# Kernel tuning notes

Hardware: AMD Instinct MI355X
Metric: run time of the kernel (lower is better)

## Reference

```python
import jax, jax.numpy as jnp
import numpy as np

Q, N, D = 4096, 100000, 128


def setup_inputs() -> dict:
    key = jax.random.key(0)
    k1, k2, k3 = jax.random.split(key, 3)
    inputs = jax.random.normal(k1, (Q, D), dtype=jnp.float32)
    X_train = jax.random.normal(k2, (N, D), dtype=jnp.float32)
    y_train = jax.random.normal(k3, (N,), dtype=jnp.float32)
    return {"inputs": inputs, "X_train": X_train, "y_train": y_train, "k": 32}


def reference(inputs, X_train, y_train, k):
    # Squared Euclidean distances [Q, N] via the expanded identity
    # |a-b|^2 = |a|^2 + |b|^2 - 2 a.b  (avoids materializing [Q, N, D]).
    q_sq = jnp.sum(inputs * inputs, axis=-1, keepdims=True)        # [Q, 1]
    t_sq = jnp.sum(X_train * X_train, axis=-1)                     # [N]
    cross = jnp.einsum('qd,nd->qn', inputs, X_train)               # [Q, N]
    distances = q_sq + t_sq[None, :] - 2.0 * cross                 # [Q, N]
    # top_k of -distances == k nearest neighbors
    _, indices = jax.lax.top_k(-distances, k)                      # [Q, k]
    nearest = y_train[indices]                                     # [Q, k]
    return jnp.mean(nearest, axis=1)                               # [Q]
```

## Files before the change

### kernel.cpp

```cpp
#include <hip/hip_runtime.h>
#include <hip/hip_fp16.h>
#include <cstdint>
#include <cstddef>


constexpr int Q_  = 4096;
constexpr int N_  = 100000;
constexpr int D_  = 128;
constexpr int K_  = 32;

constexpr int QT    = 32;
constexpr int BN    = 256;
constexpr int NCH   = 8;
constexpr int CHUNK = 12544;
constexpr int ITERS = CHUNK / BN;
constexpr int NPAD  = NCH * CHUNK;
constexpr int CW    = 128;
constexpr int QTS   = 16;
constexpr int SAMP_M      = 8192;
constexpr int SAMP_STRIDE = 12;
constexpr int SAMP_OFF    = 5;
constexpr int SAMP_ITERS  = SAMP_M / BN;

constexpr int XS_B  = NPAD / 64;
constexpr int SAM_B = SAMP_M / 64;
constexpr int PQ_B  = Q_ / 4;
constexpr int MXN   = XS_B * 4;

typedef __attribute__((ext_vector_type(8))) _Float16 half8;
typedef __attribute__((ext_vector_type(4))) float    floatx4;
typedef unsigned long long ull;

#define DEV __device__ __forceinline__
constexpr ull DEADC = ~0ull;

DEV ull pack_cand(float score, unsigned int n) {
    unsigned int s = __float_as_uint(score);
    s = (s & 0x80000000u) ? ~s : (s | 0x80000000u);
    return ((ull)s << 32) | (ull)n;
}
DEV float unpack_score(ull k) {
    unsigned int s = (unsigned int)(k >> 32);
    s = (s & 0x80000000u) ? (s ^ 0x80000000u) : ~s;
    return __uint_as_float(s);
}
DEV ull u64min(ull a, ull b) { return a < b ? a : b; }
DEV float inf_f() { return __int_as_float(0x7f800000); }

DEV ull bitonic64(ull v, int L) {
    #pragma unroll
    for (int k2 = 2; k2 <= 64; k2 <<= 1)
        #pragma unroll
        for (int j2 = k2 >> 1; j2 >= 1; j2 >>= 1) {
            ull o = __shfl_xor(v, j2);
            bool up = ((L & k2) == 0);
            bool lo = ((L & j2) == 0);
            ull mn = u64min(v, o), mx = v ^ o ^ mn;
            v = (lo == up) ? mn : mx;
        }
    return v;
}
DEV ull bimerge64(ull v, int L) {
    #pragma unroll
    for (int j2 = 32; j2 >= 1; j2 >>= 1) {
        ull o = __shfl_xor(v, j2);
        ull mn = u64min(v, o), mx = v ^ o ^ mn;
        v = ((L & j2) == 0) ? mn : mx;
    }
    return v;
}

__global__ void prep_all(const float* __restrict__ X, const float* __restrict__ Qm,
                         __half* __restrict__ Xs, float* __restrict__ tsq,
                         float* __restrict__ mxArr, float* __restrict__ mxArrH,
                         __half* __restrict__ Xsam, float* __restrict__ tsqS,
                         __half* __restrict__ Qh,
                         float* __restrict__ qsq, float* __restrict__ qrs,
                         int* __restrict__ flagF)
{
    const int tid = threadIdx.x, L = tid & 63, wv = tid >> 6;
    const int bx = blockIdx.x;
    const int am = L & 15, aq = L >> 4;

    if (bx < XS_B) {
        int t16 = bx * 4 + wv;
        int r = t16 * 16 + am;
        float ssq = 0.f, xr2 = 0.f, xh2 = 0.f;
        #pragma unroll
        for (int ks = 0; ks < 4; ++ks) {
            int c = ks * 32 + aq * 8;
            float v0=0,v1=0,v2=0,v3=0,v4=0,v5=0,v6=0,v7=0;
            if (r < N_) {
                float4 a = *(const float4*)(X + (size_t)r * D_ + c);
                float4 b = *(const float4*)(X + (size_t)r * D_ + c + 4);
                v0=a.x; v1=a.y; v2=a.z; v3=a.w; v4=b.x; v5=b.y; v6=b.z; v7=b.w;
            }
            half8 h;
            h[0]=(_Float16)v0; h[1]=(_Float16)v1; h[2]=(_Float16)v2; h[3]=(_Float16)v3;
            h[4]=(_Float16)v4; h[5]=(_Float16)v5; h[6]=(_Float16)v6; h[7]=(_Float16)v7;
            float c0=(float)h[0], c1=(float)h[1], c2=(float)h[2], c3=(float)h[3];
            float c4=(float)h[4], c5=(float)h[5], c6=(float)h[6], c7=(float)h[7];
            float r0=v0-c0, r1=v1-c1, r2=v2-c2, r3=v3-c3;
            float r4=v4-c4, r5=v5-c5, r6=v6-c6, r7=v7-c7;
            ssq += v0*v0+v1*v1+v2*v2+v3*v3+v4*v4+v5*v5+v6*v6+v7*v7;
            xr2 += r0*r0+r1*r1+r2*r2+r3*r3+r4*r4+r5*r5+r6*r6+r7*r7;
            xh2 += c0*c0+c1*c1+c2*c2+c3*c3+c4*c4+c5*c5+c6*c6+c7*c7;
            *(half8*)(Xs + ((size_t)(t16 * 4 + ks)) * 512 + L * 8) = h;
        }
        ssq += __shfl_xor(ssq, 16); ssq += __shfl_xor(ssq, 32);
        xr2 += __shfl_xor(xr2, 16); xr2 += __shfl_xor(xr2, 32);
        xh2 += __shfl_xor(xh2, 16); xh2 += __shfl_xor(xh2, 32);
        if (aq == 0) tsq[r] = (r < N_) ? ssq : inf_f();
        float m = xr2;
        m = fmaxf(m, __shfl_xor(m, 1)); m = fmaxf(m, __shfl_xor(m, 2));
        m = fmaxf(m, __shfl_xor(m, 4)); m = fmaxf(m, __shfl_xor(m, 8));
        float mh = xh2;
        mh = fmaxf(mh, __shfl_xor(mh, 1)); mh = fmaxf(mh, __shfl_xor(mh, 2));
        mh = fmaxf(mh, __shfl_xor(mh, 4)); mh = fmaxf(mh, __shfl_xor(mh, 8));
        if (L == 0) { mxArr[t16] = m; mxArrH[t16] = mh; }
    } else if (bx < XS_B + SAM_B) {
        int t16 = (bx - XS_B) * 4 + wv;
        int j = t16 * 16 + am;
        int n = j * SAMP_STRIDE + SAMP_OFF;
        float ssq = 0.f;
        #pragma unroll
        for (int ks = 0; ks < 4; ++ks) {
            int c = ks * 32 + aq * 8;
            float4 a = *(const float4*)(X + (size_t)n * D_ + c);
            float4 b = *(const float4*)(X + (size_t)n * D_ + c + 4);
            half8 h;
            h[0]=(_Float16)a.x; h[1]=(_Float16)a.y; h[2]=(_Float16)a.z; h[3]=(_Float16)a.w;
            h[4]=(_Float16)b.x; h[5]=(_Float16)b.y; h[6]=(_Float16)b.z; h[7]=(_Float16)b.w;
            ssq += a.x*a.x + a.y*a.y + a.z*a.z + a.w*a.w
                 + b.x*b.x + b.y*b.y + b.z*b.z + b.w*b.w;
            *(half8*)(Xsam + ((size_t)(t16 * 4 + ks)) * 512 + L * 8) = h;
        }
        ssq += __shfl_xor(ssq, 16); ssq += __shfl_xor(ssq, 32);
        if (aq == 0) tsqS[j] = ssq;
    } else {
        int r = (bx - XS_B - SAM_B) * 4 + wv;
        float2 x = *(const float2*)(Qm + (size_t)r * D_ + 2 * L);
        __half h0 = __float2half(x.x), h1 = __float2half(x.y);
        size_t o = (size_t)r * D_ + 2 * L;
        Qh[o] = h0; Qh[o + 1] = h1;
        float r0 = x.x - __half2float(h0), r1 = x.y - __half2float(h1);
        float s  = x.x * x.x + x.y * x.y;
        float sr = r0 * r0 + r1 * r1;
        s  += __shfl_xor(s, 32);  s += __shfl_xor(s, 16);  s += __shfl_xor(s, 8);
        s  += __shfl_xor(s, 4);   s += __shfl_xor(s, 2);   s += __shfl_xor(s, 1);
        sr += __shfl_xor(sr, 32); sr += __shfl_xor(sr, 16); sr += __shfl_xor(sr, 8);
        sr += __shfl_xor(sr, 4);  sr += __shfl_xor(sr, 2);  sr += __shfl_xor(sr, 1);
        if (L == 0) { qsq[r] = s; qrs[r] = sr; flagF[r] = 0; }
    }
}

__global__ void reduce_mx(const float* __restrict__ mxArr,
                          const float* __restrict__ mxArrH,
                          float* __restrict__ mxOut)
{
    __shared__ float sR[4], sH[4];
    const int tid = threadIdx.x, L = tid & 63, wv = tid >> 6;
    float a = 0.f, b = 0.f;
    #pragma unroll 1
    for (int i = tid; i < MXN; i += 256) {
        a = fmaxf(a, mxArr[i]);
        b = fmaxf(b, mxArrH[i]);
    }
    #pragma unroll
    for (int s = 32; s; s >>= 1) {
        a = fmaxf(a, __shfl_xor(a, s));
        b = fmaxf(b, __shfl_xor(b, s));
    }
    if (L == 0) { sR[wv] = a; sH[wv] = b; }
    __syncthreads();
    if (tid == 0) {
        mxOut[0] = fmaxf(fmaxf(sR[0], sR[1]), fmaxf(sR[2], sR[3]));
        mxOut[1] = fmaxf(fmaxf(sH[0], sH[1]), fmaxf(sH[2], sH[3]));
    }
}

__global__ __launch_bounds__(256, 2) void sample_T(
    const __half* __restrict__ Qh, const __half* __restrict__ Xsam,
    const float* __restrict__ tsqS, const float* __restrict__ qsq,
    const float* __restrict__ qrs, const float* __restrict__ mxOut,
    float* __restrict__ Teff, float* __restrict__ rawT, float* __restrict__ EwA)
{
    __shared__ float sT[QTS][130];
    const int tid = threadIdx.x, L = tid & 63, wv = tid >> 6;
    const int qbase = blockIdx.x * QTS;
    const int nwv = wv * 64;
    const int am = L & 15, aq = L >> 4;

    half8 afh[4];
    #pragma unroll
    for (int ks = 0; ks < 4; ++ks) {
        size_t o = (size_t)(qbase + am) * D_ + ks * 32 + aq * 8;
        afh[ks] = *(const half8*)(Qh + o);
    }

    float t2a[4], t2b[4];
    #pragma unroll
    for (int rg = 0; rg < 4; ++rg) { t2a[rg] = inf_f(); t2b[rg] = inf_f(); }

    const __half* bp = Xsam + (size_t)nwv * 128 + (size_t)L * 8;
    const float*  tp = tsqS + nwv + am;

    half8 bc[4], bn[4];
    #pragma unroll
    for (int nt = 0; nt < 4; ++nt)
        bc[nt] = *(const half8*)(bp + nt * 2048);

    #pragma unroll 1
    for (int it = 0; it < SAMP_ITERS; ++it) {
        float ts[4];
        #pragma unroll
        for (int nt = 0; nt < 4; ++nt) ts[nt] = tp[nt * 16];

        floatx4 acc[4] = {};
        #pragma unroll
        for (int ks = 0; ks < 4; ++ks) {
            const __half* pp = (ks < 3) ? (bp + (ks + 1) * 512) : (bp + 32768);
            #pragma unroll
            for (int nt = 0; nt < 4; ++nt)
                bn[nt] = *(const half8*)(pp + nt * 2048);
            #pragma unroll
            for (int nt = 0; nt < 4; ++nt)
                acc[nt] = __builtin_amdgcn_mfma_f32_16x16x32_f16(
                    afh[ks], bc[nt], acc[nt], 0, 0, 0);
            #pragma unroll
            for (int nt = 0; nt < 4; ++nt) bc[nt] = bn[nt];
        }
        #pragma unroll
        for (int rg = 0; rg < 4; ++rg) {
            float m1 = t2a[rg], m2 = t2b[rg];
            #pragma unroll
            for (int nt = 0; nt < 4; ++nt) {
                float v = ts[nt] - 2.f * acc[nt][rg];
                if (v < m2) { if (v < m1) { m2 = m1; m1 = v; } else m2 = v; }
            }
            t2a[rg] = m1; t2b[rg] = m2;
        }
        bp += 32768; tp += BN;
    }
    #pragma unroll
    for (int rg = 0; rg < 4; ++rg) {
        int q = aq * 4 + rg;
        sT[q][wv * 32 + am * 2 + 0] = t2a[rg];
        sT[q][wv * 32 + am * 2 + 1] = t2b[rg];
    }
    __syncthreads();

    const float mxr = mxOut[0], mxh = mxOut[1];

    #pragma unroll 1
    for (int j = 0; j < 4; ++j) {
        int q = wv * 4 + j;
        float a = sT[q][2 * L], b = sT[q][2 * L + 1];
        float g = 0.f;
        #pragma unroll 1
        for (int r = 0; r < 16; ++r) {
            float mn = fminf(a, b);
            mn = fminf(mn, __shfl_xor(mn, 32)); mn = fminf(mn, __shfl_xor(mn, 16));
            mn = fminf(mn, __shfl_xor(mn, 8));  mn = fminf(mn, __shfl_xor(mn, 4));
            mn = fminf(mn, __shfl_xor(mn, 2));  mn = fminf(mn, __shfl_xor(mn, 1));
            g = mn;
            ull ba = __ballot(a == g);
            if (ba) { if (L == __ffsll(ba) - 1) a = inf_f(); }
            else    { ull bb = __ballot(b == g); if (L == __ffsll(bb) - 1) b = inf_f(); }
        }
        if (L == 0) {
            int gq = qbase + q;
            float e = 2.f * (sqrtf(qsq[gq]) * sqrtf(mxr)
                           + sqrtf(qrs[gq]) * sqrtf(mxh)) + 0.02f;
            rawT[gq] = g; EwA[gq] = e; Teff[gq] = g + e;
        }
    }
}

__global__ __launch_bounds__(256, 4) void knn_main(
    const __half* __restrict__ Qh, const __half* __restrict__ Xs,
    const float* __restrict__ tsq, const float* __restrict__ Teff,
    ull* __restrict__ candG, int* __restrict__ cntC, int* __restrict__ flagF)
{
    __shared__ ull candL[QT][CW];
    __shared__ int cntL[QT];

    const int tid = threadIdx.x, L = tid & 63, wv = tid >> 6;
    const int lb = blockIdx.x, ch = lb & 7;
    const int qbase = (lb >> 3) * QT, chBase = ch * CHUNK, nwv = wv * 64;
    const int am = L & 15, aq = L >> 4;

    if (tid < QT) cntL[tid] = 0;
    __syncthreads();

    float th[2][4];
    float nH[2];
    #pragma unroll
    for (int qt = 0; qt < 2; ++qt) {
        #pragma unroll
        for (int rg = 0; rg < 4; ++rg)
            th[qt][rg] = Teff[qbase + qt * 16 + aq * 4 + rg];
        float m = fmaxf(fmaxf(th[qt][0], th[qt][1]), fmaxf(th[qt][2], th[qt][3]));
        nH[qt] = -0.5f * m - 1e-3f;
    }

    half8 afh[2][4];
    #pragma unroll
    for (int qt = 0; qt < 2; ++qt)
        #pragma unroll
        for (int ks = 0; ks < 4; ++ks) {
            size_t o = (size_t)(qbase + qt * 16 + am) * D_ + ks * 32 + aq * 8;
            afh[qt][ks] = *(const half8*)(Qh + o);
        }

    const __half* bp = Xs + (size_t)(chBase + nwv) * 128 + (size_t)L * 8;
    const float*  tp = tsq + chBase + nwv + am;
    int n0 = chBase + nwv + am;

    half8 bc[4], bn[4];
    #pragma unroll
    for (int nt = 0; nt < 4; ++nt)
        bc[nt] = *(const half8*)(bp + nt * 2048);

    #pragma unroll 1
    for (int it = 0; it < ITERS; ++it) {
        float ts[4];
        #pragma unroll
        for (int nt = 0; nt < 4; ++nt) ts[nt] = tp[nt * 16];

        floatx4 acc[2][4] = {};
        #pragma unroll
        for (int ks = 0; ks < 4; ++ks) {
            const __half* pp = (ks < 3) ? (bp + (ks + 1) * 512) : (bp + 32768);
            #pragma unroll
            for (int nt = 0; nt < 4; ++nt)
                bn[nt] = *(const half8*)(pp + nt * 2048);
            #pragma unroll
            for (int nt = 0; nt < 4; ++nt) {
                acc[0][nt] = __builtin_amdgcn_mfma_f32_16x16x32_f16(
                    afh[0][ks], bc[nt], acc[0][nt], 0, 0, 0);
                acc[1][nt] = __builtin_amdgcn_mfma_f32_16x16x32_f16(
                    afh[1][ks], bc[nt], acc[1][nt], 0, 0, 0);
            }
            #pragma unroll
            for (int nt = 0; nt < 4; ++nt) bc[nt] = bn[nt];
        }

        unsigned hit = 0;
        #pragma unroll
        for (int nt = 0; nt < 4; ++nt) {
            #pragma unroll
            for (int qt = 0; qt < 2; ++qt) {
                float mx = fmaxf(fmaxf(acc[qt][nt][0], acc[qt][nt][1]),
                                 fmaxf(acc[qt][nt][2], acc[qt][nt][3]));
                float Gm = fmaf(0.5f, ts[nt], nH[qt]);
                if (mx > Gm) hit |= 1u << (nt * 2 + qt);
            }
        }
        if (__any(hit != 0)) {
            #pragma unroll
            for (int nt = 0; nt < 4; ++nt) {
                #pragma unroll
                for (int qt = 0; qt < 2; ++qt) {
                    if (!__any(hit & (1u << (nt * 2 + qt)))) continue;
                    unsigned n = (unsigned)(n0 + nt * 16);
                    #pragma unroll
                    for (int rg = 0; rg < 4; ++rg) {
                        float s = fmaf(-2.f, acc[qt][nt][rg], ts[nt]);
                        if (s < th[qt][rg]) {
                            int q = qt * 16 + aq * 4 + rg;
                            int pos = atomicAdd(&cntL[q], 1);
                            if (pos < CW)
                                candL[q][pos] = pack_cand(s, n);
                            else
                                flagF[qbase + q] = 1;
                        }
                    }
                }
            }
        }
        bp += 32768; tp += BN; n0 += BN;
    }

    __syncthreads();

    #pragma unroll 1
    for (int j = 0; j < 8; ++j) {
        int q = wv * 8 + j;
        int gq = qbase + q;
        int c = cntL[q];
        int cc = c < CW ? c : CW;
        ull* dst = candG + ((size_t)gq * NCH + ch) * CW;
        #pragma unroll
        for (int off = 0; off < CW; off += 64)
            if (off + L < cc) dst[off + L] = candL[q][off + L];
        if (L == 0) cntC[gq * NCH + ch] = cc;
    }
}

__global__ void finalize(const ull* __restrict__ candG, const int* __restrict__ cntC,
                         const int* __restrict__ flagF, const float* __restrict__ Qm,
                         const float* __restrict__ X, const float* __restrict__ tsq,
                         const float* __restrict__ rawT, const float* __restrict__ EwA,
                         const float* __restrict__ Ytr, float* __restrict__ out)
{
    __shared__ ull fb[4][256];
    int L = threadIdx.x & 63;
    int wv = threadIdx.x >> 6;
    int q = blockIdx.x * 4 + wv;
    bool bad = (flagF[q] != 0);
    float result = 0.f;

    if (!bad) {
        int cg = (L < NCH) ? cntC[q * NCH + L] : 0;
        int ctot = cg;
        ctot += __shfl_xor(ctot, 32); ctot += __shfl_xor(ctot, 16);
        ctot += __shfl_xor(ctot, 8);  ctot += __shfl_xor(ctot, 4);
        ctot += __shfl_xor(ctot, 2);  ctot += __shfl_xor(ctot, 1);
        if (ctot < K_) bad = true;
        else {
            ull s = DEADC;
            #pragma unroll 1
            for (int g = 0; g < NCH; ++g) {
                int c_g = __shfl(cg, g);
                const ull* cb = candG + ((size_t)q * NCH + g) * CW;
                #pragma unroll 1
                for (int off = 0; off < c_g; off += 64) {
                    ull v = (off + L < c_g) ? cb[off + L] : DEADC;
                    v = bitonic64(v, L);
                    ull w = __shfl(v, 63 - L);
                    s = bimerge64(u64min(s, w), L);
                }
            }
            int cr = ctot < 64 ? ctot : 64;
            unsigned n = (unsigned)(s & 0xffffffffu);
            ull pe = DEADC;
            if (L < cr) {
                const float4* xp = (const float4*)(X + (size_t)n * D_);
                const float4* qp = (const float4*)(Qm + (size_t)q * D_);
                float d = 0.f;
                #pragma unroll 8
                for (int i = 0; i < 32; ++i) {
                    float4 xv = xp[i], qv = qp[i];
                    d += qv.x * xv.x + qv.y * xv.y + qv.z * xv.z + qv.w * xv.w;
                }
                pe = pack_cand(tsq[n] - 2.f * d, n);
            }
            ull pe2 = bitonic64(pe, L);
            float exact31 = unpack_score(__shfl(pe2, K_ - 1));
            bool ok = exact31 < rawT[q];
            if (ctot > 64) {
                float A63 = unpack_score(__shfl(s, 63));
                ok = ok && (A63 - EwA[q] > exact31);
            }
            if (!ok) bad = true;
            else {
                float ys = 0.f;
                if (L < K_) ys = Ytr[(unsigned)(pe2 & 0xffffffffu)];
                ys += __shfl_xor(ys, 32); ys += __shfl_xor(ys, 16);
                ys += __shfl_xor(ys, 8);  ys += __shfl_xor(ys, 4);
                ys += __shfl_xor(ys, 2);  ys += __shfl_xor(ys, 1);
                result = ys * (1.f / K_);
            }
        }
    }

    if (bad) {
        const float4* qp = (const float4*)(Qm + (size_t)q * D_);
        float T = rawT[q] + EwA[q];
        float lo = 0.f, hi = 0.f;
        bool haveLo = false, haveHi = false;
        int cnt = 0;
        #pragma unroll 1
        for (int att = 0; att < 40; ++att) {
            cnt = 0;
            #pragma unroll 1
            for (int j = 0; j < NPAD / 64; ++j) {
                int n = j * 64 + L;
                float s = inf_f();
                if (n < N_) {
                    const float4* xp = (const float4*)(X + (size_t)n * D_);
                    float d = 0.f;
                    #pragma unroll 4
                    for (int i = 0; i < 32; ++i) {
                        float4 xv = xp[i], qv = qp[i];
                        d += qv.x * xv.x + qv.y * xv.y + qv.z * xv.z + qv.w * xv.w;
                    }
                    s = tsq[n] - 2.f * d;
                }
                bool want = s < T;
                ull m = __ballot(want);
                if (m) {
                    int pos = cnt + (int)__popcll(m & ((1ull << L) - 1ull));
                    if (want && pos < 256) fb[wv][pos] = pack_cand(s, (unsigned)n);
                    cnt += (int)__popcll(m);
                }
            }
            if (cnt >= K_ && cnt <= 256) break;
            if (cnt < K_) { lo = T; haveLo = true;
                T = haveHi ? 0.5f * (T + hi) : T + exp2f((float)att) * 0.5f; }
            else { hi = T; haveHi = true;
                T = haveLo ? 0.5f * (lo + T) : T - exp2f((float)att) * 0.5f; }
        }
        if (cnt >= K_ && cnt <= 256) {
            ull s64 = DEADC;
            #pragma unroll 1
            for (int off = 0; off < 256; off += 64) {
                if (off >= cnt) break;
                ull v = (off + L < cnt) ? fb[wv][off + L] : DEADC;
                v = bitonic64(v, L);
                ull w = __shfl(v, 63 - L);
                s64 = bimerge64(u64min(s64, w), L);
            }
            float ys = (L < K_) ? Ytr[(unsigned)(s64 & 0xffffffffu)] : 0.f;
            ys += __shfl_xor(ys, 32); ys += __shfl_xor(ys, 16);
            ys += __shfl_xor(ys, 8);  ys += __shfl_xor(ys, 4);
            ys += __shfl_xor(ys, 2);  ys += __shfl_xor(ys, 1);
            result = ys * (1.f / K_);
        } else {
            ull last = 0;
            float ysum = 0.f;
            for (int r = 0; r < K_; ++r) {
                ull best = DEADC;
                for (int j = 0; j < NPAD / 64; ++j) {
                    int n = j * 64 + L;
                    if (n < N_) {
                        const float4* xp = (const float4*)(X + (size_t)n * D_);
                        float d = 0.f;
                        #pragma unroll 4
                        for (int i = 0; i < 32; ++i) {
                            float4 xv = xp[i], qv = qp[i];
                            d += qv.x * xv.x + qv.y * xv.y + qv.z * xv.z + qv.w * xv.w;
                        }
                        ull k = pack_cand(tsq[n] - 2.f * d, n);
                        if (k > last && k < best) best = k;
                    }
                }
                best = u64min(best, __shfl_xor(best, 32));
                best = u64min(best, __shfl_xor(best, 16));
                best = u64min(best, __shfl_xor(best, 8));
                best = u64min(best, __shfl_xor(best, 4));
                best = u64min(best, __shfl_xor(best, 2));
                best = u64min(best, __shfl_xor(best, 1));
                if (L == 0) ysum += Ytr[(unsigned)(best & 0xffffffffu)];
                last = best;
            }
            result = ysum * (1.f / K_);
        }
    }
    if (L == 0) out[q] = result;
}

extern "C" void kernel_launch(void* const* d_in, const int* in_sizes, int n_in,
                              void* d_out, int out_size, void* d_ws, size_t ws_size,
                              hipStream_t stream)
{
    const float* Qm  = (const float*)d_in[0];
    const float* X   = (const float*)d_in[1];
    const float* Ytr = (const float*)d_in[2];
    float* out = (float*)d_out;

    char* w = (char*)d_ws;
    auto alloc = [&](size_t bytes) {
        char* p = w; w += (bytes + 255) & ~(size_t)255; return p;
    };
    __half* Xs   = (__half*)  alloc((size_t)(NPAD + BN) * D_ * 2);
    __half* Qh   = (__half*)  alloc((size_t)Q_ * D_ * 2);
    float*  ts   = (float*)   alloc((size_t)NPAD * 4);
    __half* Xsm  = (__half*)  alloc((size_t)(SAMP_M + BN) * D_ * 2);
    float*  tsS  = (float*)   alloc((size_t)SAMP_M * 4);
    ull*    cd   = (ull*)     alloc((size_t)Q_ * NCH * CW * 8);
    int*    cnC  = (int*)     alloc((size_t)Q_ * NCH * 4);
    int*    flg  = (int*)     alloc((size_t)Q_ * 4);
    float*  mxA  = (float*)   alloc((size_t)MXN * 4);
    float*  mxAH = (float*)   alloc((size_t)MXN * 4);
    float*  mxO  = (float*)   alloc(256);
    float*  Tef  = (float*)   alloc((size_t)Q_ * 4);
    float*  rwT  = (float*)   alloc((size_t)Q_ * 4);
    float*  Ew   = (float*)   alloc((size_t)Q_ * 4);
    float*  qs   = (float*)   alloc((size_t)Q_ * 4);
    float*  qr2  = (float*)   alloc((size_t)Q_ * 4);

    prep_all<<<XS_B + SAM_B + PQ_B, 256, 0, stream>>>(
        X, Qm, Xs, ts, mxA, mxAH, Xsm, tsS, Qh, qs, qr2, flg);
    reduce_mx<<<1, 256, 0, stream>>>(mxA, mxAH, mxO);
    sample_T<<<Q_ / QTS, 256, 0, stream>>>(Qh, Xsm, tsS, qs, qr2, mxO,
                                           Tef, rwT, Ew);
    knn_main<<<(Q_ / QT) * NCH, 256, 0, stream>>>(Qh, Xs, ts, Tef, cd, cnC, flg);
    finalize<<<Q_ / 4, 256, 0, stream>>>(cd, cnC, flg, Qm, X, ts, rwT, Ew, Ytr, out);
}
```

Measured before the change: 455.3 us.

## Stage train tiles in LDS with double buffering and 64-query blocks

The main distance kernel now processes 64 queries per block, with each wave owning 16 queries. The four waves share one 64-row tile of train vectors that is double-buffered in LDS and prefetched through registers. Before, each wave streamed its own train columns straight from global memory for 32 queries, so this raises reuse of each loaded train row. The local candidate buffer shrinks to 56 entries, and overflow up to 128 spills directly to global memory. In exchange, every iteration adds a block-wide barrier, and occupancy drops to 2 blocks per CU.

```diff
diff --git a/kernel.cpp b/kernel.cpp
--- a/kernel.cpp
+++ b/kernel.cpp
@@ -9,18 +9,19 @@
 constexpr int D_  = 128;
 constexpr int K_  = 32;
 
-constexpr int QT    = 32;
-constexpr int BN    = 256;
+constexpr int QT    = 64;
+constexpr int TN    = 64;
 constexpr int NCH   = 8;
 constexpr int CHUNK = 12544;
-constexpr int ITERS = CHUNK / BN;
+constexpr int KITERS = CHUNK / TN;
 constexpr int NPAD  = NCH * CHUNK;
 constexpr int CW    = 128;
+constexpr int CWL   = 56;
 constexpr int QTS   = 16;
 constexpr int SAMP_M      = 8192;
 constexpr int SAMP_STRIDE = 12;
 constexpr int SAMP_OFF    = 5;
-constexpr int SAMP_ITERS  = SAMP_M / BN;
+constexpr int SAMP_ITERS  = SAMP_M / 256;
 
 constexpr int XS_B  = NPAD / 64;
 constexpr int SAM_B = SAMP_M / 64;
@@ -240,7 +241,7 @@
             }
             t2a[rg] = m1; t2b[rg] = m2;
         }
-        bp += 32768; tp += BN;
+        bp += 32768; tp += 256;
     }
     #pragma unroll
     for (int rg = 0; rg < 4; ++rg) {
@@ -277,123 +278,124 @@
     }
 }
 
-__global__ __launch_bounds__(256, 4) void knn_main(
+__global__ __launch_bounds__(256, 2) void knn_main(
     const __half* __restrict__ Qh, const __half* __restrict__ Xs,
     const float* __restrict__ tsq, const float* __restrict__ Teff,
     ull* __restrict__ candG, int* __restrict__ cntC, int* __restrict__ flagF)
 {
-    __shared__ ull candL[QT][CW];
+    __shared__ __half bufA[2][TN * D_];
+    __shared__ ull candL[QT][CWL];
     __shared__ int cntL[QT];
 
     const int tid = threadIdx.x, L = tid & 63, wv = tid >> 6;
     const int lb = blockIdx.x, ch = lb & 7;
-    const int qbase = (lb >> 3) * QT, chBase = ch * CHUNK, nwv = wv * 64;
+    const int qbase = (lb >> 3) * QT, chBase = ch * CHUNK;
     const int am = L & 15, aq = L >> 4;
 
     if (tid < QT) cntL[tid] = 0;
+
+    float th[4];
+    #pragma unroll
+    for (int rg = 0; rg < 4; ++rg)
+        th[rg] = Teff[qbase + wv * 16 + aq * 4 + rg];
+    float maxTh = fmaxf(fmaxf(th[0], th[1]), fmaxf(th[2], th[3]));
+    maxTh = fmaxf(maxTh, __shfl_xor(maxTh, 16));
+    maxTh = fmaxf(maxTh, __shfl_xor(maxTh, 32));
+    const float nH = -0.5f * maxTh - 1e-3f;
+
+    half8 afh[4];
+    #pragma unroll
+    for (int ks = 0; ks < 4; ++ks) {
+        size_t o = (size_t)(qbase + wv * 16 + am) * D_ + ks * 32 + aq * 8;
+        afh[ks] = *(const half8*)(Qh + o);
+    }
+
+    const __half* src = Xs + (size_t)chBase * D_ + tid * 8;
+    const float*  tp  = tsq + chBase + am;
+
+    half8 st[4];
+    #pragma unroll
+    for (int r = 0; r < 4; ++r)
+        st[r] = *(const half8*)(src + r * 2048);
+    #pragma unroll
+    for (int r = 0; r < 4; ++r)
+        *(half8*)(&bufA[0][r * 2048 + tid * 8]) = st[r];
+    #pragma unroll
+    for (int r = 0; r < 4; ++r)
+        st[r] = *(const half8*)(src + 8192 + r * 2048);
+    const __half* srcp = src + 16384;
     __syncthreads();
 
-    float th[2][4];
-    float nH[2];
-    #pragma unroll
-    for (int qt = 0; qt < 2; ++qt) {
-        #pragma unroll
-        for (int rg = 0; rg < 4; ++rg)
-            th[qt][rg] = Teff[qbase + qt * 16 + aq * 4 + rg];
-        float m = fmaxf(fmaxf(th[qt][0], th[qt][1]), fmaxf(th[qt][2], th[qt][3]));
-        nH[qt] = -0.5f * m - 1e-3f;
-    }
-
-    half8 afh[2][4];
-    #pragma unroll
-    for (int qt = 0; qt < 2; ++qt)
-        #pragma unroll
-        for (int ks = 0; ks < 4; ++ks) {
-            size_t o = (size_t)(qbase + qt * 16 + am) * D_ + ks * 32 + aq * 8;
-            afh[qt][ks] = *(const half8*)(Qh + o);
-        }
-
-    const __half* bp = Xs + (size_t)(chBase + nwv) * 128 + (size_t)L * 8;
-    const float*  tp = tsq + chBase + nwv + am;
-    int n0 = chBase + nwv + am;
-
-    half8 bc[4], bn[4];
-    #pragma unroll
-    for (int nt = 0; nt < 4; ++nt)
-        bc[nt] = *(const half8*)(bp + nt * 2048);
-
     #pragma unroll 1
-    for (int it = 0; it < ITERS; ++it) {
+    for (int it = 0; it < KITERS; ++it) {
+        const __half* bb = &bufA[it & 1][0];
         float ts[4];
         #pragma unroll
-        for (int nt = 0; nt < 4; ++nt) ts[nt] = tp[nt * 16];
-
-        floatx4 acc[2][4] = {};
-        #pragma unroll
-        for (int ks = 0; ks < 4; ++ks) {
-            const __half* pp = (ks < 3) ? (bp + (ks + 1) * 512) : (bp + 32768);
-            #pragma unroll
-            for (int nt = 0; nt < 4; ++nt)
-                bn[nt] = *(const half8*)(pp + nt * 2048);
+        for (int nt = 0; nt < 4; ++nt) ts[nt] = tp[it * TN + nt * 16];
+
+        floatx4 acc[4] = {};
+        #pragma unroll
+        for (int ks = 0; ks < 4; ++ks)
             #pragma unroll
             for (int nt = 0; nt < 4; ++nt) {
-                acc[0][nt] = __builtin_amdgcn_mfma_f32_16x16x32_f16(
-                    afh[0][ks], bc[nt], acc[0][nt], 0, 0, 0);
-                acc[1][nt] = __builtin_amdgcn_mfma_f32_16x16x32_f16(
-                    afh[1][ks], bc[nt], acc[1][nt], 0, 0, 0);
-            }
-            #pragma unroll
-            for (int nt = 0; nt < 4; ++nt) bc[nt] = bn[nt];
-        }
+                half8 b = *(const half8*)(bb + (nt * 4 + ks) * 512 + L * 8);
+                acc[nt] = __builtin_amdgcn_mfma_f32_16x16x32_f16(
+                    afh[ks], b, acc[nt], 0, 0, 0);
+            }
 
         unsigned hit = 0;
         #pragma unroll
         for (int nt = 0; nt < 4; ++nt) {
-            #pragma unroll
-            for (int qt = 0; qt < 2; ++qt) {
-                float mx = fmaxf(fmaxf(acc[qt][nt][0], acc[qt][nt][1]),
-                                 fmaxf(acc[qt][nt][2], acc[qt][nt][3]));
-                float Gm = fmaf(0.5f, ts[nt], nH[qt]);
-                if (mx > Gm) hit |= 1u << (nt * 2 + qt);
-            }
+            float mx = fmaxf(fmaxf(acc[nt][0], acc[nt][1]),
+                             fmaxf(acc[nt][2], acc[nt][3]));
+            float Gm = fmaf(0.5f, ts[nt], nH);
+            if (mx > Gm) hit |= 1u << nt;
         }
         if (__any(hit != 0)) {
             #pragma unroll
             for (int nt = 0; nt < 4; ++nt) {
+                if (!__any(hit & (1u << nt))) continue;
+                unsigned n = (unsigned)(chBase + it * TN + nt * 16 + am);
                 #pragma unroll
-                for (int qt = 0; qt < 2; ++qt) {
-                    if (!__any(hit & (1u << (nt * 2 + qt)))) continue;
-                    unsigned n = (unsigned)(n0 + nt * 16);
-                    #pragma unroll
-                    for (int rg = 0; rg < 4; ++rg) {
-                        float s = fmaf(-2.f, acc[qt][nt][rg], ts[nt]);
-                        if (s < th[qt][rg]) {
-                            int q = qt * 16 + aq * 4 + rg;
-                            int pos = atomicAdd(&cntL[q], 1);
-                            if (pos < CW)
-                                candL[q][pos] = pack_cand(s, n);
-                            else
-                                flagF[qbase + q] = 1;
-                        }
+                for (int rg = 0; rg < 4; ++rg) {
+                    float s = fmaf(-2.f, acc[nt][rg], ts[nt]);
+                    if (s < th[rg]) {
+                        int q = wv * 16 + aq * 4 + rg;
+                        int pos = atomicAdd(&cntL[q], 1);
+                        if (pos < CWL)
+                            candL[q][pos] = pack_cand(s, n);
+                        else if (pos < CW)
+                            candG[((size_t)(qbase + q) * NCH + ch) * CW + pos]
+                                = pack_cand(s, n);
+                        else
+                            flagF[qbase + q] = 1;
                     }
                 }
             }
         }
-        bp += 32768; tp += BN; n0 += BN;
-    }
-
-    __syncthreads();
+
+        {
+            __half* wb = &bufA[(it + 1) & 1][0];
+            #pragma unroll
+            for (int r = 0; r < 4; ++r)
+                *(half8*)(wb + r * 2048 + tid * 8) = st[r];
+            #pragma unroll
+            for (int r = 0; r < 4; ++r)
+                st[r] = *(const half8*)(srcp + r * 2048);
+            srcp += 8192;
+        }
+        __syncthreads();
+    }
 
     #pragma unroll 1
-    for (int j = 0; j < 8; ++j) {
-        int q = wv * 8 + j;
+    for (int j = 0; j < 16; ++j) {
+        int q = wv * 16 + j;
         int gq = qbase + q;
         int c = cntL[q];
         int cc = c < CW ? c : CW;
+        int ccl = c < CWL ? c : CWL;
         ull* dst = candG + ((size_t)gq * NCH + ch) * CW;
-        #pragma unroll
-        for (int off = 0; off < CW; off += 64)
-            if (off + L < cc) dst[off + L] = candL[q][off + L];
+        if (L < ccl) dst[L] = candL[q][L];
         if (L == 0) cntC[gq * NCH + ch] = cc;
     }
 }
@@ -564,10 +566,10 @@
     auto alloc = [&](size_t bytes) {
         char* p = w; w += (bytes + 255) & ~(size_t)255; return p;
     };
-    __half* Xs   = (__half*)  alloc((size_t)(NPAD + BN) * D_ * 2);
+    __half* Xs   = (__half*)  alloc((size_t)(NPAD + 256) * D_ * 2);
     __half* Qh   = (__half*)  alloc((size_t)Q_ * D_ * 2);
     float*  ts   = (float*)   alloc((size_t)NPAD * 4);
-    __half* Xsm  = (__half*)  alloc((size_t)(SAMP_M + BN) * D_ * 2);
+    __half* Xsm  = (__half*)  alloc((size_t)(SAMP_M + 256) * D_ * 2);
     float*  tsS  = (float*)   alloc((size_t)SAMP_M * 4);
     ull*    cd   = (ull*)     alloc((size_t)Q_ * NCH * CW * 8);
     int*    cnC  = (int*)     alloc((size_t)Q_ * NCH * 4);
```

Result: slower. 475.6 us (+4.5%).
